# Performance work log

Hardware: AMD Instinct MI355X
Metric: run time of the kernel (lower is better)

## Reference

```python
import jax, jax.numpy as jnp
import numpy as np

HID = 64
ENC_T = 20
DEC_T = 30


def lstm_cell(x, h, c, W_ih, W_hh, b_ih, b_hh):
    # PyTorch LSTMCell gate order: i, f, g, o
    gates = x @ W_ih.T + h @ W_hh.T + b_ih + b_hh  # [B, 4*HID]
    i, f, g, o = jnp.split(gates, 4, axis=-1)
    c_new = jax.nn.sigmoid(f) * c + jax.nn.sigmoid(i) * jnp.tanh(g)
    h_new = jax.nn.sigmoid(o) * jnp.tanh(c_new)
    return h_new, c_new


def setup_inputs() -> dict:
    key = jax.random.key(0)
    ks = jax.random.split(key, 11)
    B = 65536
    s_enc = 1.0 / np.sqrt(HID)
    u = lambda k, shape: jax.random.uniform(k, shape, jnp.float32, -s_enc, s_enc)
    return {
        "train_traj": jax.random.normal(ks[0], (B, ENC_T, 2), jnp.float32),
        "W_ih_enc": u(ks[1], (4 * HID, 2)),
        "W_hh_enc": u(ks[2], (4 * HID, HID)),
        "b_ih_enc": u(ks[3], (4 * HID,)),
        "b_hh_enc": u(ks[4], (4 * HID,)),
        "W_ih_dec": u(ks[5], (4 * HID, HID)),
        "W_hh_dec": u(ks[6], (4 * HID, HID)),
        "b_ih_dec": u(ks[7], (4 * HID,)),
        "b_hh_dec": u(ks[8], (4 * HID,)),
        "W_pos": u(ks[9], (2, HID)),
        "b_pos": u(ks[10], (2,)),
    }


def reference(train_traj, W_ih_enc, W_hh_enc, b_ih_enc, b_hh_enc,
              W_ih_dec, W_hh_dec, b_ih_dec, b_hh_dec, W_pos, b_pos):
    B = train_traj.shape[0]
    h0 = jnp.zeros((B, HID), train_traj.dtype)
    c0 = jnp.zeros((B, HID), train_traj.dtype)

    # Encoder: scan over the 20 time steps
    def enc_step(carry, x_t):
        h, c = carry
        h, c = lstm_cell(x_t, h, c, W_ih_enc, W_hh_enc, b_ih_enc, b_hh_enc)
        return (h, c), None

    xs = jnp.transpose(train_traj, (1, 0, 2))  # [T, B, 2]
    (h, c), _ = jax.lax.scan(enc_step, (h0, c0), xs)

    # Decoder: feed h back in as the input for 30 steps
    def dec_step(carry, _):
        h, c = carry
        h_new, c_new = lstm_cell(h, h, c, W_ih_dec, W_hh_dec, b_ih_dec, b_hh_dec)
        out = h_new @ W_pos.T + b_pos  # [B, 2]
        return (h_new, c_new), out

    (_, _), outs = jax.lax.scan(dec_step, (h, c), None, length=DEC_T)
    return jnp.transpose(outs, (1, 0, 2))  # [B, 30, 2]
```

## Files before the change

kernel.cpp:

```cpp
#include <hip/hip_runtime.h>

#define HID   64
#define ENC_T 20
#define DEC_T 30
#define ROWS  32
#define HS    72

typedef _Float16 f16;
typedef _Float16 f16x8 __attribute__((ext_vector_type(8)));
typedef _Float16 f16x4 __attribute__((ext_vector_type(4)));
typedef float  f32x4  __attribute__((ext_vector_type(4)));
typedef float  f32x2  __attribute__((ext_vector_type(2)));
typedef unsigned int   uint_t;

#if __has_builtin(__builtin_amdgcn_exp2f)
#define EXP2F(x) __builtin_amdgcn_exp2f(x)
#else
#define EXP2F(x) exp2f(x)
#endif
#if __has_builtin(__builtin_amdgcn_rcpf)
#define RCPF(x) __builtin_amdgcn_rcpf(x)
#else
#define RCPF(x) (1.0f / (x))
#endif

#define L2E 1.4426950408889634f

__device__ __forceinline__ f32x2 exp2_2(f32x2 x) {
    f32x2 r; r[0] = EXP2F(x[0]); r[1] = EXP2F(x[1]); return r;
}
__device__ __forceinline__ void batch_inv4_pk(f32x2 D0, f32x2 D1, f32x2 D2, f32x2 D3,
                                              f32x2& i0, f32x2& i1, f32x2& i2, f32x2& i3) {
    f32x2 m01 = D0 * D1;
    f32x2 m23 = D2 * D3;
    f32x2 p   = m01 * m23;
    f32x2 r;
    r[0] = RCPF(p[0]);
    r[1] = RCPF(p[1]);
    f32x2 r01 = r * m23;
    f32x2 r23 = r * m01;
    i0 = r01 * D1;
    i1 = r01 * D0;
    i2 = r23 * D3;
    i3 = r23 * D2;
}
__device__ __forceinline__ f32x4 batch_inv4(float D0, float D1, float D2, float D3) {
    float m01 = D0 * D1;
    float m23 = D2 * D3;
    float r   = RCPF(m01 * m23);
    float r01 = r * m23;
    float r23 = r * m01;
    f32x4 o;
    o[0] = r01 * D1;
    o[1] = r01 * D0;
    o[2] = r23 * D3;
    o[3] = r23 * D2;
    return o;
}

__device__ __forceinline__ f16x8 load8h(const float* __restrict__ p, float s) {
    f16x8 r;
    #pragma unroll
    for (int u = 0; u < 8; ++u) r[u] = (f16)(p[u] * s);
    return r;
}

__global__ __launch_bounds__(256, 4)
void lstm_seq2seq(const float* __restrict__ traj,
                  const float* __restrict__ WihE, const float* __restrict__ WhhE,
                  const float* __restrict__ bihE, const float* __restrict__ bhhE,
                  const float* __restrict__ WihD, const float* __restrict__ WhhD,
                  const float* __restrict__ bihD, const float* __restrict__ bhhD,
                  const float* __restrict__ Wpos, const float* __restrict__ bpos,
                  float* __restrict__ out)
{
    __shared__ __align__(16) f16   sH[2][ROWS * HS];
    __shared__ __align__(16) f16x4 sXh[ROWS * ENC_T + ENC_T];
    __shared__ __align__(16) float sP[2][ROWS * 8];

    const int tid  = threadIdx.x;
    const int w    = tid >> 6;
    const int lane = tid & 63;
    const int col  = lane & 15;
    const int quad = lane >> 4;
    const int wg   = blockIdx.x;

    const float gsc[4] = { L2E, L2E, 2.0f * L2E, L2E };

    {
        const float* src = traj + (size_t)wg * (ROWS * ENC_T * 2);
        for (int p = tid; p < ROWS * ENC_T; p += 256) {
            f32x2 xp = *(const f32x2*)(src + 2 * p);
            f16 xh0 = (f16)xp[0], xh1 = (f16)xp[1];
            f16x4 v;
            v[0] = xh0; v[1] = xh1;
            v[2] = (f16)(xp[0] - (float)xh0);
            v[3] = (f16)(xp[1] - (float)xh1);
            sXh[p] = v;
        }
        if (tid < ENC_T) {
            f16x4 zz = {};
            sXh[ROWS * ENC_T + tid] = zz;
        }
    }
    {
        uint_t* hz = (uint_t*)&sH[0][0];
        for (int j = tid; j < ROWS * HS / 2; j += 256) hz[j] = 0;
    }

    f16x8 bw[4][3];
    #pragma unroll
    for (int j = 0; j < 4; ++j) {
        int g = 64 * j + 16 * w + col;
        #pragma unroll
        for (int kb = 0; kb < 2; ++kb)
            bw[j][kb] = load8h(WhhE + g * 64 + kb * 32 + quad * 8, gsc[j]);
        float w0 = WihE[g * 2 + 0] * gsc[j];
        float w1 = WihE[g * 2 + 1] * gsc[j];
        float bs = (bihE[g] + bhhE[g]) * gsc[j];
        f16 w0h = (f16)w0, w1h = (f16)w1, bh = (f16)bs;
        f16 w0l = (f16)(w0 - (float)w0h);
        f16 w1l = (f16)(w1 - (float)w1h);
        f16 bl  = (f16)(bs - (float)bh);
        f16x8 a2 = {};
        if (quad == 0) {
            a2[0] = w0h; a2[1] = w1h; a2[2] = w0l; a2[3] = w1l; a2[4] = bh; a2[5] = bl;
        }
        bw[j][2] = a2;
    }

    const uint_t onesd = (quad == 0) ? 0x3C003C00u : 0u;
    const int xbase0 = (quad == 0) ? (col      * ENC_T) : (ROWS * ENC_T);
    const int xbase1 = (quad == 0) ? ((col+16) * ENC_T) : (ROWS * ENC_T);
    const f32x4 z4 = { 0.f, 0.f, 0.f, 0.f };

    const f32x2 one2  = { 1.f, 1.f };
    const f32x2 two2  = { 2.f, 2.f };
    const f32x2 mone2 = { -1.f, -1.f };
    const f32x2 msc2  = { -2.f * L2E, -2.f * L2E };

    f32x2 c2[2][2] = {{{0.f,0.f},{0.f,0.f}},{{0.f,0.f},{0.f,0.f}}};
    int buf = 0;

    __syncthreads();

    for (int t = 0; t < ENC_T; ++t) {
        #pragma unroll
        for (int g = 0; g < 2; ++g) {
            const int colg = col + 16 * g;
            union { f16x4 v; uint_t d[2]; } xfu;
            xfu.v = sXh[(g ? xbase1 : xbase0) + t];
            union { f16x8 v; uint_t d[4]; } b2u;
            b2u.d[0] = xfu.d[0];
            b2u.d[1] = xfu.d[1];
            b2u.d[2] = onesd;
            b2u.d[3] = 0;
            f16x8 b0 = *(const f16x8*)&sH[buf][colg * HS +  0 + quad * 8];
            f16x8 b1 = *(const f16x8*)&sH[buf][colg * HS + 32 + quad * 8];
            f32x4 acc[4];
            #pragma unroll
            for (int j = 0; j < 4; ++j) {
                acc[j] = __builtin_amdgcn_mfma_f32_16x16x32_f16(bw[j][2], b2u.v, z4, 0, 0, 0);
                acc[j] = __builtin_amdgcn_mfma_f32_16x16x32_f16(bw[j][0], b0, acc[j], 0, 0, 0);
                acc[j] = __builtin_amdgcn_mfma_f32_16x16x32_f16(bw[j][1], b1, acc[j], 0, 0, 0);
            }
            f32x2 so2[2], cn2[2];
            #pragma unroll
            for (int rp = 0; rp < 2; ++rp) {
                f32x2 a0 = { acc[0][2*rp], acc[0][2*rp+1] };
                f32x2 a1 = { acc[1][2*rp], acc[1][2*rp+1] };
                f32x2 a2v = { acc[2][2*rp], acc[2][2*rp+1] };
                f32x2 a3 = { acc[3][2*rp], acc[3][2*rp+1] };
                f32x2 i0, i1, i2, i3;
                batch_inv4_pk(exp2_2(-a0) + one2, exp2_2(-a1) + one2,
                              exp2_2(-a2v) + one2, exp2_2(-a3) + one2,
                              i0, i1, i2, i3);
                f32x2 tg = __builtin_elementwise_fma(two2, i2, mone2);
                f32x2 cn = __builtin_elementwise_fma(i1, c2[g][rp], i0 * tg);
                c2[g][rp] = cn;
                cn2[rp] = cn;
                so2[rp] = i3;
            }
            float Dc[4];
            #pragma unroll
            for (int rp = 0; rp < 2; ++rp) {
                f32x2 xs = cn2[rp] * msc2;
                Dc[2*rp+0] = 1.f + EXP2F(fminf(fmaxf(xs[0], -30.f), 30.f));
                Dc[2*rp+1] = 1.f + EXP2F(fminf(fmaxf(xs[1], -30.f), 30.f));
            }
            f32x4 invc = batch_inv4(Dc[0], Dc[1], Dc[2], Dc[3]);
            f16x4 hh;
            #pragma unroll
            for (int rp = 0; rp < 2; ++rp) {
                f32x2 ic = { invc[2*rp], invc[2*rp+1] };
                f32x2 th = __builtin_elementwise_fma(two2, ic, mone2);
                f32x2 hn = so2[rp] * th;
                hh[2*rp+0] = (f16)hn[0];
                hh[2*rp+1] = (f16)hn[1];
            }
            *(f16x4*)&sH[buf ^ 1][colg * HS + 16 * w + quad * 4] = hh;
        }
        __syncthreads();
        buf ^= 1;
    }

    f32x4 bD4[4];
    #pragma unroll
    for (int j = 0; j < 4; ++j) {
        int g = 64 * j + 16 * w + col;
        #pragma unroll
        for (int kb = 0; kb < 2; ++kb) {
            int off = g * 64 + kb * 32 + quad * 8;
            float tmp[8];
            #pragma unroll
            for (int u = 0; u < 8; ++u) tmp[u] = WihD[off + u] + WhhD[off + u];
            bw[j][kb] = load8h(tmp, gsc[j]);
        }
        #pragma unroll
        for (int r = 0; r < 4; ++r) {
            int gr = 64 * j + 16 * w + quad * 4 + r;
            bD4[j][r] = (bihD[gr] + bhhD[gr]) * gsc[j];
        }
    }

    f32x2 wpA2[2], wpB2[2];
    #pragma unroll
    for (int rp = 0; rp < 2; ++rp) {
        int u = 16 * w + quad * 4 + 2 * rp;
        wpA2[rp][0] = Wpos[u];       wpA2[rp][1] = Wpos[u + 1];
        wpB2[rp][0] = Wpos[64 + u];  wpB2[rp][1] = Wpos[64 + u + 1];
    }
    const int   rrow  = w * 8 + (lane >> 1);
    const int   rcomp = lane & 1;
    const float bp    = bpos[rcomp];

    for (int t = 0; t < DEC_T; ++t) {
        #pragma unroll
        for (int g = 0; g < 2; ++g) {
            const int colg = col + 16 * g;
            f16x8 b0 = *(const f16x8*)&sH[buf][colg * HS +  0 + quad * 8];
            f16x8 b1 = *(const f16x8*)&sH[buf][colg * HS + 32 + quad * 8];
            f32x4 acc[4];
            #pragma unroll
            for (int j = 0; j < 4; ++j) {
                acc[j] = __builtin_amdgcn_mfma_f32_16x16x32_f16(bw[j][0], b0, bD4[j], 0, 0, 0);
                acc[j] = __builtin_amdgcn_mfma_f32_16x16x32_f16(bw[j][1], b1, acc[j], 0, 0, 0);
            }
            f32x2 so2[2], cn2[2];
            #pragma unroll
            for (int rp = 0; rp < 2; ++rp) {
                f32x2 a0 = { acc[0][2*rp], acc[0][2*rp+1] };
                f32x2 a1 = { acc[1][2*rp], acc[1][2*rp+1] };
                f32x2 a2v = { acc[2][2*rp], acc[2][2*rp+1] };
                f32x2 a3 = { acc[3][2*rp], acc[3][2*rp+1] };
                f32x2 i0, i1, i2, i3;
                batch_inv4_pk(exp2_2(-a0) + one2, exp2_2(-a1) + one2,
                              exp2_2(-a2v) + one2, exp2_2(-a3) + one2,
                              i0, i1, i2, i3);
                f32x2 tg = __builtin_elementwise_fma(two2, i2, mone2);
                f32x2 cn = __builtin_elementwise_fma(i1, c2[g][rp], i0 * tg);
                c2[g][rp] = cn;
                cn2[rp] = cn;
                so2[rp] = i3;
            }
            float Dc[4];
            #pragma unroll
            for (int rp = 0; rp < 2; ++rp) {
                f32x2 xs = cn2[rp] * msc2;
                Dc[2*rp+0] = 1.f + EXP2F(fminf(fmaxf(xs[0], -30.f), 30.f));
                Dc[2*rp+1] = 1.f + EXP2F(fminf(fmaxf(xs[1], -30.f), 30.f));
            }
            f32x4 invc = batch_inv4(Dc[0], Dc[1], Dc[2], Dc[3]);
            f16x4 hh;
            f32x2 pA = { 0.f, 0.f }, pB = { 0.f, 0.f };
            #pragma unroll
            for (int rp = 0; rp < 2; ++rp) {
                f32x2 ic = { invc[2*rp], invc[2*rp+1] };
                f32x2 th = __builtin_elementwise_fma(two2, ic, mone2);
                f32x2 hn = so2[rp] * th;
                pA = __builtin_elementwise_fma(hn, wpA2[rp], pA);
                pB = __builtin_elementwise_fma(hn, wpB2[rp], pB);
                hh[2*rp+0] = (f16)hn[0];
                hh[2*rp+1] = (f16)hn[1];
            }
            *(f16x4*)&sH[buf ^ 1][colg * HS + 16 * w + quad * 4] = hh;
            float p0 = pA[0] + pA[1];
            float p1 = pB[0] + pB[1];
            p0 += __shfl_xor(p0, 16, 64);
            p0 += __shfl_xor(p0, 32, 64);
            p1 += __shfl_xor(p1, 16, 64);
            p1 += __shfl_xor(p1, 32, 64);
            if (quad == 0) {
                sP[buf ^ 1][colg * 8 + 0 + w] = p0;
                sP[buf ^ 1][colg * 8 + 4 + w] = p1;
            }
        }
        __syncthreads();
        buf ^= 1;
        if (lane < 16) {
            f32x4 v = *(const f32x4*)&sP[buf][rrow * 8 + rcomp * 4];
            float p = (v[0] + v[1]) + (v[2] + v[3]) + bp;
            out[(size_t)(wg * ROWS + rrow) * (DEC_T * 2) + t * 2 + rcomp] = p;
        }
    }
}

extern "C" void kernel_launch(void* const* d_in, const int* in_sizes, int n_in,
                              void* d_out, int out_size, void* d_ws, size_t ws_size,
                              hipStream_t stream) {
    const float* traj = (const float*)d_in[0];
    const float* WihE = (const float*)d_in[1];
    const float* WhhE = (const float*)d_in[2];
    const float* bihE = (const float*)d_in[3];
    const float* bhhE = (const float*)d_in[4];
    const float* WihD = (const float*)d_in[5];
    const float* WhhD = (const float*)d_in[6];
    const float* bihD = (const float*)d_in[7];
    const float* bhhD = (const float*)d_in[8];
    const float* Wpos = (const float*)d_in[9];
    const float* bpos = (const float*)d_in[10];
    float* out = (float*)d_out;

    const int B = in_sizes[0] / (ENC_T * 2);
    const int grid = B / ROWS;

    lstm_seq2seq<<<grid, 256, 0, stream>>>(traj, WihE, WhhE, bihE, bhhE,
                                           WihD, WhhD, bihD, bhhD, Wpos, bpos, out);
}
```

Measured before the change: 316.7 us.

## Halve block to two waves, each computing two 16-unit hidden slices

Each block now runs 2 waves instead of 4, and each wave handles 32 hidden units as two 16-unit sub-tiles, keeping twice as many weight fragments in registers. The block still covers 32 rows. Fewer waves per block means a cheaper barrier each step, and each h fragment read from shared memory is reused for twice as many MFMAs. The cost is higher register pressure (launch bounds 128,2) and fewer waves per CU to hide latency. The per-step projection partials and the output write indexing are adjusted for 2 waves.

```diff
diff --git a/kernel.cpp b/kernel.cpp
--- a/kernel.cpp
+++ b/kernel.cpp
@@ -5,6 +5,7 @@
 #define DEC_T 30
 #define ROWS  32
 #define HS    72
+
 
 typedef _Float16 f16;
 typedef _Float16 f16x8 __attribute__((ext_vector_type(8)));
@@ -65,7 +66,7 @@
     return r;
 }
 
-__global__ __launch_bounds__(256, 4)
+__global__ __launch_bounds__(128, 2)
 void lstm_seq2seq(const float* __restrict__ traj,
                   const float* __restrict__ WihE, const float* __restrict__ WhhE,
                   const float* __restrict__ bihE, const float* __restrict__ bhhE,
@@ -76,7 +77,7 @@
 {
     __shared__ __align__(16) f16   sH[2][ROWS * HS];
     __shared__ __align__(16) f16x4 sXh[ROWS * ENC_T + ENC_T];
-    __shared__ __align__(16) float sP[2][ROWS * 8];
+    __shared__ __align__(16) float sP[2][ROWS * 4];
 
     const int tid  = threadIdx.x;
     const int w    = tid >> 6;
@@ -89,7 +90,7 @@
 
     {
         const float* src = traj + (size_t)wg * (ROWS * ENC_T * 2);
-        for (int p = tid; p < ROWS * ENC_T; p += 256) {
+        for (int p = tid; p < ROWS * ENC_T; p += 128) {
             f32x2 xp = *(const f32x2*)(src + 2 * p);
             f16 xh0 = (f16)xp[0], xh1 = (f16)xp[1];
             f16x4 v;
@@ -105,29 +106,31 @@
     }
     {
         uint_t* hz = (uint_t*)&sH[0][0];
-        for (int j = tid; j < ROWS * HS / 2; j += 256) hz[j] = 0;
+        for (int j = tid; j < ROWS * HS / 2; j += 128) hz[j] = 0;
     }
 
-    f16x8 bw[4][3];
+    f16x8 bw[4][2][3];
     #pragma unroll
-    for (int j = 0; j < 4; ++j) {
-        int g = 64 * j + 16 * w + col;
-        #pragma unroll
-        for (int kb = 0; kb < 2; ++kb)
-            bw[j][kb] = load8h(WhhE + g * 64 + kb * 32 + quad * 8, gsc[j]);
-        float w0 = WihE[g * 2 + 0] * gsc[j];
-        float w1 = WihE[g * 2 + 1] * gsc[j];
-        float bs = (bihE[g] + bhhE[g]) * gsc[j];
-        f16 w0h = (f16)w0, w1h = (f16)w1, bh = (f16)bs;
-        f16 w0l = (f16)(w0 - (float)w0h);
-        f16 w1l = (f16)(w1 - (float)w1h);
-        f16 bl  = (f16)(bs - (float)bh);
-        f16x8 a2 = {};
-        if (quad == 0) {
-            a2[0] = w0h; a2[1] = w1h; a2[2] = w0l; a2[3] = w1l; a2[4] = bh; a2[5] = bl;
-        }
-        bw[j][2] = a2;
-    }
+    for (int j = 0; j < 4; ++j)
+        #pragma unroll
+        for (int st = 0; st < 2; ++st) {
+            int g = 64 * j + 32 * w + 16 * st + col;
+            #pragma unroll
+            for (int kb = 0; kb < 2; ++kb)
+                bw[j][st][kb] = load8h(WhhE + g * 64 + kb * 32 + quad * 8, gsc[j]);
+            float w0 = WihE[g * 2 + 0] * gsc[j];
+            float w1 = WihE[g * 2 + 1] * gsc[j];
+            float bs = (bihE[g] + bhhE[g]) * gsc[j];
+            f16 w0h = (f16)w0, w1h = (f16)w1, bh = (f16)bs;
+            f16 w0l = (f16)(w0 - (float)w0h);
+            f16 w1l = (f16)(w1 - (float)w1h);
+            f16 bl  = (f16)(bs - (float)bh);
+            f16x8 a2 = {};
+            if (quad == 0) {
+                a2[0] = w0h; a2[1] = w1h; a2[2] = w0l; a2[3] = w1l; a2[4] = bh; a2[5] = bl;
+            }
+            bw[j][st][2] = a2;
+        }
 
     const uint_t onesd = (quad == 0) ? 0x3C003C00u : 0u;
     const int xbase0 = (quad == 0) ? (col      * ENC_T) : (ROWS * ENC_T);
@@ -139,7 +142,7 @@
     const f32x2 mone2 = { -1.f, -1.f };
     const f32x2 msc2  = { -2.f * L2E, -2.f * L2E };
 
-    f32x2 c2[2][2] = {{{0.f,0.f},{0.f,0.f}},{{0.f,0.f},{0.f,0.f}}};
+    f32x2 c2[2][2][2] = {};
     int buf = 0;
 
     __syncthreads();
@@ -157,80 +160,87 @@
             b2u.d[3] = 0;
             f16x8 b0 = *(const f16x8*)&sH[buf][colg * HS +  0 + quad * 8];
             f16x8 b1 = *(const f16x8*)&sH[buf][colg * HS + 32 + quad * 8];
-            f32x4 acc[4];
-            #pragma unroll
-            for (int j = 0; j < 4; ++j) {
-                acc[j] = __builtin_amdgcn_mfma_f32_16x16x32_f16(bw[j][2], b2u.v, z4, 0, 0, 0);
-                acc[j] = __builtin_amdgcn_mfma_f32_16x16x32_f16(bw[j][0], b0, acc[j], 0, 0, 0);
-                acc[j] = __builtin_amdgcn_mfma_f32_16x16x32_f16(bw[j][1], b1, acc[j], 0, 0, 0);
-            }
-            f32x2 so2[2], cn2[2];
-            #pragma unroll
-            for (int rp = 0; rp < 2; ++rp) {
-                f32x2 a0 = { acc[0][2*rp], acc[0][2*rp+1] };
-                f32x2 a1 = { acc[1][2*rp], acc[1][2*rp+1] };
-                f32x2 a2v = { acc[2][2*rp], acc[2][2*rp+1] };
-                f32x2 a3 = { acc[3][2*rp], acc[3][2*rp+1] };
-                f32x2 i0, i1, i2, i3;
-                batch_inv4_pk(exp2_2(-a0) + one2, exp2_2(-a1) + one2,
-                              exp2_2(-a2v) + one2, exp2_2(-a3) + one2,
-                              i0, i1, i2, i3);
-                f32x2 tg = __builtin_elementwise_fma(two2, i2, mone2);
-                f32x2 cn = __builtin_elementwise_fma(i1, c2[g][rp], i0 * tg);
-                c2[g][rp] = cn;
-                cn2[rp] = cn;
-                so2[rp] = i3;
-            }
-            float Dc[4];
-            #pragma unroll
-            for (int rp = 0; rp < 2; ++rp) {
-                f32x2 xs = cn2[rp] * msc2;
-                Dc[2*rp+0] = 1.f + EXP2F(fminf(fmaxf(xs[0], -30.f), 30.f));
-                Dc[2*rp+1] = 1.f + EXP2F(fminf(fmaxf(xs[1], -30.f), 30.f));
-            }
-            f32x4 invc = batch_inv4(Dc[0], Dc[1], Dc[2], Dc[3]);
-            f16x4 hh;
-            #pragma unroll
-            for (int rp = 0; rp < 2; ++rp) {
-                f32x2 ic = { invc[2*rp], invc[2*rp+1] };
-                f32x2 th = __builtin_elementwise_fma(two2, ic, mone2);
-                f32x2 hn = so2[rp] * th;
-                hh[2*rp+0] = (f16)hn[0];
-                hh[2*rp+1] = (f16)hn[1];
-            }
-            *(f16x4*)&sH[buf ^ 1][colg * HS + 16 * w + quad * 4] = hh;
+            #pragma unroll
+            for (int st = 0; st < 2; ++st) {
+                f32x4 acc[4];
+                #pragma unroll
+                for (int j = 0; j < 4; ++j) {
+                    acc[j] = __builtin_amdgcn_mfma_f32_16x16x32_f16(bw[j][st][2], b2u.v, z4, 0, 0, 0);
+                    acc[j] = __builtin_amdgcn_mfma_f32_16x16x32_f16(bw[j][st][0], b0, acc[j], 0, 0, 0);
+                    acc[j] = __builtin_amdgcn_mfma_f32_16x16x32_f16(bw[j][st][1], b1, acc[j], 0, 0, 0);
+                }
+                f32x2 so2[2], cn2[2];
+                #pragma unroll
+                for (int rp = 0; rp < 2; ++rp) {
+                    f32x2 a0 = { acc[0][2*rp], acc[0][2*rp+1] };
+                    f32x2 a1 = { acc[1][2*rp], acc[1][2*rp+1] };
+                    f32x2 a2v = { acc[2][2*rp], acc[2][2*rp+1] };
+                    f32x2 a3 = { acc[3][2*rp], acc[3][2*rp+1] };
+                    f32x2 i0, i1, i2, i3;
+                    batch_inv4_pk(exp2_2(-a0) + one2, exp2_2(-a1) + one2,
+                                  exp2_2(-a2v) + one2, exp2_2(-a3) + one2,
+                                  i0, i1, i2, i3);
+                    f32x2 tg = __builtin_elementwise_fma(two2, i2, mone2);
+                    f32x2 cn = __builtin_elementwise_fma(i1, c2[g][st][rp], i0 * tg);
+                    c2[g][st][rp] = cn;
+                    cn2[rp] = cn;
+                    so2[rp] = i3;
+                }
+                float Dc[4];
+                #pragma unroll
+                for (int rp = 0; rp < 2; ++rp) {
+                    f32x2 xs = cn2[rp] * msc2;
+                    Dc[2*rp+0] = 1.f + EXP2F(fminf(fmaxf(xs[0], -30.f), 30.f));
+                    Dc[2*rp+1] = 1.f + EXP2F(fminf(fmaxf(xs[1], -30.f), 30.f));
+                }
+                f32x4 invc = batch_inv4(Dc[0], Dc[1], Dc[2], Dc[3]);
+                f16x4 hh;
+                #pragma unroll
+                for (int rp = 0; rp < 2; ++rp) {
+                    f32x2 ic = { invc[2*rp], invc[2*rp+1] };
+                    f32x2 th = __builtin_elementwise_fma(two2, ic, mone2);
+                    f32x2 hn = so2[rp] * th;
+                    hh[2*rp+0] = (f16)hn[0];
+                    hh[2*rp+1] = (f16)hn[1];
+                }
+                *(f16x4*)&sH[buf ^ 1][colg * HS + 32 * w + 16 * st + quad * 4] = hh;
+            }
         }
         __syncthreads();
         buf ^= 1;
     }
 
-    f32x4 bD4[4];
+    f32x4 bD4[4][2];
     #pragma unroll
-    for (int j = 0; j < 4; ++j) {
-        int g = 64 * j + 16 * w + col;
-        #pragma unroll
-        for (int kb = 0; kb < 2; ++kb) {
-            int off = g * 64 + kb * 32 + quad * 8;
-            float tmp[8];
-            #pragma unroll
-            for (int u = 0; u < 8; ++u) tmp[u] = WihD[off + u] + WhhD[off + u];
-            bw[j][kb] = load8h(tmp, gsc[j]);
-        }
-        #pragma unroll
-        for (int r = 0; r < 4; ++r) {
-            int gr = 64 * j + 16 * w + quad * 4 + r;
-            bD4[j][r] = (bihD[gr] + bhhD[gr]) * gsc[j];
-        }
-    }
-
-    f32x2 wpA2[2], wpB2[2];
+    for (int j = 0; j < 4; ++j)
+        #pragma unroll
+        for (int st = 0; st < 2; ++st) {
+            int g = 64 * j + 32 * w + 16 * st + col;
+            #pragma unroll
+            for (int kb = 0; kb < 2; ++kb) {
+                int off = g * 64 + kb * 32 + quad * 8;
+                float tmp[8];
+                #pragma unroll
+                for (int u = 0; u < 8; ++u) tmp[u] = WihD[off + u] + WhhD[off + u];
+                bw[j][st][kb] = load8h(tmp, gsc[j]);
+            }
+            #pragma unroll
+            for (int r = 0; r < 4; ++r) {
+                int gr = 64 * j + 32 * w + 16 * st + quad * 4 + r;
+                bD4[j][st][r] = (bihD[gr] + bhhD[gr]) * gsc[j];
+            }
+        }
+
+    f32x2 wpA2[2][2], wpB2[2][2];
     #pragma unroll
-    for (int rp = 0; rp < 2; ++rp) {
-        int u = 16 * w + quad * 4 + 2 * rp;
-        wpA2[rp][0] = Wpos[u];       wpA2[rp][1] = Wpos[u + 1];
-        wpB2[rp][0] = Wpos[64 + u];  wpB2[rp][1] = Wpos[64 + u + 1];
-    }
-    const int   rrow  = w * 8 + (lane >> 1);
+    for (int st = 0; st < 2; ++st)
+        #pragma unroll
+        for (int rp = 0; rp < 2; ++rp) {
+            int u = 32 * w + 16 * st + quad * 4 + 2 * rp;
+            wpA2[st][rp][0] = Wpos[u];       wpA2[st][rp][1] = Wpos[u + 1];
+            wpB2[st][rp][0] = Wpos[64 + u];  wpB2[st][rp][1] = Wpos[64 + u + 1];
+        }
+    const int   rrow  = w * 16 + (lane >> 1);
     const int   rcomp = lane & 1;
     const float bp    = bpos[rcomp];
 
@@ -240,50 +250,53 @@
             const int colg = col + 16 * g;
             f16x8 b0 = *(const f16x8*)&sH[buf][colg * HS +  0 + quad * 8];
             f16x8 b1 = *(const f16x8*)&sH[buf][colg * HS + 32 + quad * 8];
-            f32x4 acc[4];
-            #pragma unroll
-            for (int j = 0; j < 4; ++j) {
-                acc[j] = __builtin_amdgcn_mfma_f32_16x16x32_f16(bw[j][0], b0, bD4[j], 0, 0, 0);
-                acc[j] = __builtin_amdgcn_mfma_f32_16x16x32_f16(bw[j][1], b1, acc[j], 0, 0, 0);
-            }
-            f32x2 so2[2], cn2[2];
-            #pragma unroll
-            for (int rp = 0; rp < 2; ++rp) {
-                f32x2 a0 = { acc[0][2*rp], acc[0][2*rp+1] };
-                f32x2 a1 = { acc[1][2*rp], acc[1][2*rp+1] };
-                f32x2 a2v = { acc[2][2*rp], acc[2][2*rp+1] };
-                f32x2 a3 = { acc[3][2*rp], acc[3][2*rp+1] };
-                f32x2 i0, i1, i2, i3;
-                batch_inv4_pk(exp2_2(-a0) + one2, exp2_2(-a1) + one2,
-                              exp2_2(-a2v) + one2, exp2_2(-a3) + one2,
-                              i0, i1, i2, i3);
-                f32x2 tg = __builtin_elementwise_fma(two2, i2, mone2);
-                f32x2 cn = __builtin_elementwise_fma(i1, c2[g][rp], i0 * tg);
-                c2[g][rp] = cn;
-                cn2[rp] = cn;
-                so2[rp] = i3;
-            }
-            float Dc[4];
-            #pragma unroll
-            for (int rp = 0; rp < 2; ++rp) {
-                f32x2 xs = cn2[rp] * msc2;
-                Dc[2*rp+0] = 1.f + EXP2F(fminf(fmaxf(xs[0], -30.f), 30.f));
-                Dc[2*rp+1] = 1.f + EXP2F(fminf(fmaxf(xs[1], -30.f), 30.f));
-            }
-            f32x4 invc = batch_inv4(Dc[0], Dc[1], Dc[2], Dc[3]);
-            f16x4 hh;
             f32x2 pA = { 0.f, 0.f }, pB = { 0.f, 0.f };
             #pragma unroll
-            for (int rp = 0; rp < 2; ++rp) {
-                f32x2 ic = { invc[2*rp], invc[2*rp+1] };
-                f32x2 th = __builtin_elementwise_fma(two2, ic, mone2);
-                f32x2 hn = so2[rp] * th;
-                pA = __builtin_elementwise_fma(hn, wpA2[rp], pA);
-                pB = __builtin_elementwise_fma(hn, wpB2[rp], pB);
-                hh[2*rp+0] = (f16)hn[0];
-                hh[2*rp+1] = (f16)hn[1];
-            }
-            *(f16x4*)&sH[buf ^ 1][colg * HS + 16 * w + quad * 4] = hh;
+            for (int st = 0; st < 2; ++st) {
+                f32x4 acc[4];
+                #pragma unroll
+                for (int j = 0; j < 4; ++j) {
+                    acc[j] = __builtin_amdgcn_mfma_f32_16x16x32_f16(bw[j][st][0], b0, bD4[j][st], 0, 0, 0);
+                    acc[j] = __builtin_amdgcn_mfma_f32_16x16x32_f16(bw[j][st][1], b1, acc[j], 0, 0, 0);
+                }
+                f32x2 so2[2], cn2[2];
+                #pragma unroll
+                for (int rp = 0; rp < 2; ++rp) {
+                    f32x2 a0 = { acc[0][2*rp], acc[0][2*rp+1] };
+                    f32x2 a1 = { acc[1][2*rp], acc[1][2*rp+1] };
+                    f32x2 a2v = { acc[2][2*rp], acc[2][2*rp+1] };
+                    f32x2 a3 = { acc[3][2*rp], acc[3][2*rp+1] };
+                    f32x2 i0, i1, i2, i3;
+                    batch_inv4_pk(exp2_2(-a0) + one2, exp2_2(-a1) + one2,
+                                  exp2_2(-a2v) + one2, exp2_2(-a3) + one2,
+                                  i0, i1, i2, i3);
+                    f32x2 tg = __builtin_elementwise_fma(two2, i2, mone2);
+                    f32x2 cn = __builtin_elementwise_fma(i1, c2[g][st][rp], i0 * tg);
+                    c2[g][st][rp] = cn;
+                    cn2[rp] = cn;
+                    so2[rp] = i3;
+                }
+                float Dc[4];
+                #pragma unroll
+                for (int rp = 0; rp < 2; ++rp) {
+                    f32x2 xs = cn2[rp] * msc2;
+                    Dc[2*rp+0] = 1.f + EXP2F(fminf(fmaxf(xs[0], -30.f), 30.f));
+                    Dc[2*rp+1] = 1.f + EXP2F(fminf(fmaxf(xs[1], -30.f), 30.f));
+                }
+                f32x4 invc = batch_inv4(Dc[0], Dc[1], Dc[2], Dc[3]);
+                f16x4 hh;
+                #pragma unroll
+                for (int rp = 0; rp < 2; ++rp) {
+                    f32x2 ic = { invc[2*rp], invc[2*rp+1] };
+                    f32x2 th = __builtin_elementwise_fma(two2, ic, mone2);
+                    f32x2 hn = so2[rp] * th;
+                    pA = __builtin_elementwise_fma(hn, wpA2[st][rp], pA);
+                    pB = __builtin_elementwise_fma(hn, wpB2[st][rp], pB);
+                    hh[2*rp+0] = (f16)hn[0];
+                    hh[2*rp+1] = (f16)hn[1];
+                }
+                *(f16x4*)&sH[buf ^ 1][colg * HS + 32 * w + 16 * st + quad * 4] = hh;
+            }
             float p0 = pA[0] + pA[1];
             float p1 = pB[0] + pB[1];
             p0 += __shfl_xor(p0, 16, 64);
@@ -291,15 +304,15 @@
             p1 += __shfl_xor(p1, 16, 64);
             p1 += __shfl_xor(p1, 32, 64);
             if (quad == 0) {
-                sP[buf ^ 1][colg * 8 + 0 + w] = p0;
-                sP[buf ^ 1][colg * 8 + 4 + w] = p1;
+                sP[buf ^ 1][colg * 4 + 0 + w] = p0;
+                sP[buf ^ 1][colg * 4 + 2 + w] = p1;
             }
         }
         __syncthreads();
         buf ^= 1;
-        if (lane < 16) {
-            f32x4 v = *(const f32x4*)&sP[buf][rrow * 8 + rcomp * 4];
-            float p = (v[0] + v[1]) + (v[2] + v[3]) + bp;
+        if (lane < 32) {
+            f32x2 v = *(const f32x2*)&sP[buf][rrow * 4 + rcomp * 2];
+            float p = v[0] + v[1] + bp;
             out[(size_t)(wg * ROWS + rrow) * (DEC_T * 2) + t * 2 + rcomp] = p;
         }
     }
@@ -324,6 +337,6 @@
     const int B = in_sizes[0] / (ENC_T * 2);
     const int grid = B / ROWS;
 
-    lstm_seq2seq<<<grid, 256, 0, stream>>>(traj, WihE, WhhE, bihE, bhhE,
+    lstm_seq2seq<<<grid, 128, 0, stream>>>(traj, WihE, WhhE, bihE, bhhE,
                                            WihD, WhhD, bihD, bhhD, Wpos, bpos, out);
 }
```

Result: slower. 342.2 us (+8.0%).
